# Performance work log

Hardware: AMD Instinct MI355X
Metric: run time of the kernel (lower is better)

Reference implementation:

```python
import jax, jax.numpy as jnp
import numpy as np

N, E, D, H, OUT, L, G = 50000, 800000, 128, 128, 128, 5, 512
EMB = L * H  # 640
BN_EPS = 1e-5


def setup_inputs() -> dict:
    key = jax.random.key(0)
    ks = jax.random.split(key, 24)
    s_h = 1.0 / np.sqrt(H)
    s_e = 1.0 / np.sqrt(EMB)
    inp = {
        'x': jax.random.normal(ks[0], (N, D), jnp.float32),
        'edge_index': jax.random.randint(ks[1], (2, E), 0, N, jnp.int32),
        'batch': jnp.sort(jax.random.randint(ks[2], (N,), 0, G, jnp.int32)),
        # per-layer GINConv MLP: Linear(D/H->H), BN(H), ReLU, Linear(H->H). D==H so stackable.
        'conv_W1': jax.random.normal(ks[3], (L, H, H), jnp.float32) * s_h,
        'conv_b1': jnp.zeros((L, H), jnp.float32),
        'conv_g1': jnp.ones((L, H), jnp.float32),
        'conv_be1': jnp.zeros((L, H), jnp.float32),
        'conv_W2': jax.random.normal(ks[4], (L, H, H), jnp.float32) * s_h,
        'conv_b2': jnp.zeros((L, H), jnp.float32),
        'eps': jnp.zeros((L,), jnp.float32),  # train_eps=True, init 0.0
        # outer BatchNorm per layer
        'bn_g': jnp.ones((L, H), jnp.float32),
        'bn_b': jnp.zeros((L, H), jnp.float32),
        # per-layer prediction heads Linear(H -> OUT)
        'pred_W': jax.random.normal(ks[5], (L, H, OUT), jnp.float32) * s_h,
        'pred_b': jnp.zeros((L, OUT), jnp.float32),
        # global_d FF(EMB): 3 stacked Linear(EMB,EMB) + shortcut
        'gW': jax.random.normal(ks[6], (3, EMB, EMB), jnp.float32) * s_e,
        'gb': jnp.zeros((3, EMB), jnp.float32),
        'gsW': jax.random.normal(ks[7], (EMB, EMB), jnp.float32) * s_e,
        'gsb': jnp.zeros((EMB,), jnp.float32),
        # local_d FF(EMB)
        'lW': jax.random.normal(ks[8], (3, EMB, EMB), jnp.float32) * s_e,
        'lb': jnp.zeros((3, EMB), jnp.float32),
        'lsW': jax.random.normal(ks[9], (EMB, EMB), jnp.float32) * s_e,
        'lsb': jnp.zeros((EMB,), jnp.float32),
    }
    return inp


def _bn(h, g, b):
    # BatchNorm1d, training mode: batch stats over node dim (biased var)
    m = jnp.mean(h, axis=0)
    v = jnp.var(h, axis=0)
    return g * (h - m) * jax.lax.rsqrt(v + BN_EPS) + b


def _ff(x, W, b, Ws, bs):
    h = x
    for i in range(3):
        h = jax.nn.relu(h @ W[i] + b[i])
    return h + x @ Ws + bs


def reference(x, edge_index, batch, conv_W1, conv_b1, conv_g1, conv_be1,
              conv_W2, conv_b2, eps, bn_g, bn_b, pred_W, pred_b,
              gW, gb, gsW, gsb, lW, lb, lsW, lsb):
    src, dst = edge_index[0], edge_index[1]
    h = x
    xs = []
    for i in range(L):
        # GINConv: (1+eps)*x_i + sum_{j->i} x_j, then MLP
        agg = jax.ops.segment_sum(h[src], dst, num_segments=N)
        h = (1.0 + eps[i]) * h + agg
        h = _bn(h @ conv_W1[i] + conv_b1[i], conv_g1[i], conv_be1[i])
        h = jax.nn.relu(h)
        h = h @ conv_W2[i] + conv_b2[i]
        h = jax.nn.relu(_bn(h, bn_g[i], bn_b[i]))
        xs.append(h)
    # per-layer graph sum-pool + prediction head (dropout in eval = identity)
    xpool = [jax.ops.segment_sum(xs[i], batch, num_segments=G) @ pred_W[i] + pred_b[i]
             for i in range(L)]
    xcat = jnp.concatenate(xpool, axis=1)            # [G, L*OUT]
    graph_embedding = _ff(xcat, gW, gb, gsW, gsb)     # [G, EMB]
    node_embedding = _ff(jnp.concatenate(xs, axis=1), lW, lb, lsW, lsb)  # [N, EMB]
    return (graph_embedding, node_embedding, xcat)
```

## Files before the change

### kernel.cpp

```cpp
#include <hip/hip_runtime.h>

constexpr int H    = 128;
constexpr int LNUM = 5;
constexpr int NG   = 512;
constexpr int EMB  = 640;
constexpr float BN_EPS = 1e-5f;

typedef __attribute__((ext_vector_type(8))) short bf16x8;
typedef __attribute__((ext_vector_type(4))) float f32x4;

__device__ inline unsigned short f2bf(float f){
  unsigned u = __builtin_bit_cast(unsigned, f);
  u += 0x7FFF + ((u >> 16) & 1);
  return (unsigned short)(u >> 16);
}
__device__ inline float bf2f(unsigned short h){
  unsigned u = ((unsigned)h) << 16;
  return __builtin_bit_cast(float, u);
}

__device__ inline int xcd_swz(int bid, int nwg){
  int q = nwg >> 3, r = nwg & 7;
  int xcd = bid & 7, idx = bid >> 3;
  return (xcd < r ? xcd*(q+1) : r*(q+1) + (xcd-r)*q) + idx;
}

__global__ void k_zerof(float* p, int n){
  int i = blockIdx.x*256 + threadIdx.x;
  if (i < n) p[i] = 0.f;
}
__global__ void k_zeroi(int* p, int n){
  int i = blockIdx.x*256 + threadIdx.x;
  if (i < n) p[i] = 0;
}

__global__ void k_hist(const int* __restrict__ dst, int E, int* deg){
  int e = blockIdx.x*256 + threadIdx.x;
  if (e < E) atomicAdd(&deg[dst[e]], 1);
}

__global__ __launch_bounds__(1024) void k_scan(int* degcur, int* __restrict__ rowptr, int n){
  __shared__ int wsum[16];
  __shared__ int carry;
  int tid = threadIdx.x, wid = tid >> 6, lane = tid & 63;
  if (tid == 0){ carry = 0; rowptr[0] = 0; }
  __syncthreads();
  for (int base = 0; base < n; base += 1024){
    int v = (base + tid < n) ? degcur[base + tid] : 0;
    int s = v;
#pragma unroll
    for (int off = 1; off < 64; off <<= 1){
      int t = __shfl_up(s, off);
      if (lane >= off) s += t;
    }
    if (lane == 63) wsum[wid] = s;
    __syncthreads();
    if (wid == 0 && lane < 16){
      int wv = wsum[lane];
#pragma unroll
      for (int off = 1; off < 16; off <<= 1){
        int t = __shfl_up(wv, off);
        if (lane >= off) wv += t;
      }
      wsum[lane] = wv;
    }
    __syncthreads();
    int incl = s + (wid ? wsum[wid-1] : 0) + carry;
    if (base + tid < n){ rowptr[base + tid + 1] = incl; degcur[base + tid] = incl - v; }
    __syncthreads();
    if (tid == 0) carry += wsum[15];
    __syncthreads();
  }
}

__global__ void k_scatter(const int* __restrict__ src, const int* __restrict__ dst,
                          int E, int* cursor, int* __restrict__ colsrc){
  int e = blockIdx.x*256 + threadIdx.x;
  if (e < E){
    int d = dst[e];
    int pos = atomicAdd(&cursor[d], 1);
    colsrc[pos] = src[e];
  }
}

__global__ void k_gstart(const int* __restrict__ batch, int N, int* __restrict__ gstart){
  int g = blockIdx.x*256 + threadIdx.x;
  if (g <= NG){
    int lo = 0, hi = N;
    while (lo < hi){
      int mid = (lo + hi) >> 1;
      if (batch[mid] < g) lo = mid + 1; else hi = mid;
    }
    gstart[g] = lo;
  }
}

__global__ void k_castT(const float* __restrict__ W, unsigned short* __restrict__ Wt,
                        int K, int Nn, int ldt, int koff){
  __shared__ float sh[32][33];
  const size_t in_off  = (size_t)blockIdx.z * K * Nn;
  const size_t out_off = (size_t)blockIdx.z * Nn * ldt;
  int n0 = blockIdx.x*32, k0 = blockIdx.y*32;
  int tx = threadIdx.x, ty = threadIdx.y;
  for (int r = ty; r < 32; r += 8)
    sh[r][tx] = W[in_off + (size_t)(k0 + r)*Nn + n0 + tx];
  __syncthreads();
  for (int r = ty; r < 32; r += 8)
    Wt[out_off + (size_t)(n0 + r)*ldt + koff + k0 + tx] = f2bf(sh[tx][r]);
}

__global__ void k_bias2(const float* __restrict__ a, const float* __restrict__ b,
                        float* __restrict__ o){
  int i = threadIdx.x;
  o[i] = a[i] + b[i];
}

__global__ __launch_bounds__(320) void k_pool(const unsigned short* __restrict__ xall,
                                              const int* __restrict__ gstart,
                                              float* __restrict__ pooled){
  int g = blockIdx.x;
  int t = threadIdx.x;
  int n0 = gstart[g], n1 = gstart[g+1];
  float a0 = 0.f, a1 = 0.f;
  for (int n = n0; n < n1; ++n){
    unsigned u = ((const unsigned*)xall)[(size_t)n*(EMB/2) + t];
    a0 += bf2f((unsigned short)u); a1 += bf2f((unsigned short)(u >> 16));
  }
  *(float2*)(pooled + (size_t)g*EMB + 2*t) = make_float2(a0, a1);
}

__global__ __launch_bounds__(128) void k_pred(const float* __restrict__ pooled,
                                              const float* __restrict__ W,
                                              const float* __restrict__ b,
                                              float* __restrict__ xcat){
  int g = blockIdx.x, l = blockIdx.y, o = threadIdx.x;
  __shared__ float sh[128];
  sh[o] = pooled[(size_t)g*EMB + l*H + o];
  __syncthreads();
  const float* Wl = W + (size_t)l*H*H;
  float acc = b[l*H + o];
  for (int k = 0; k < H; ++k) acc = fmaf(sh[k], Wl[k*H + o], acc);
  xcat[(size_t)g*EMB + l*H + o] = acc;
}

template<bool RELU, bool OUT_BF16, bool DUAL>
__global__ __launch_bounds__(512) void k_mm(
    const unsigned short* __restrict__ A, int lda,
    const unsigned short* __restrict__ A2,
    const unsigned short* __restrict__ Bt, int ldb,
    const float* __restrict__ bias,
    void* __restrict__ Cv, int ldc,
    int M, int K)
{
  __shared__ union LdsU {
    unsigned short stage[4][8192];
    unsigned short sc16[128*136];
    float          sc32[128*132];
  } u;
  const int tid  = threadIdx.x;
  const int lane = tid & 63;
  const int w    = tid >> 6;
  const int wr   = w >> 2, wc = w & 3;

  const int nwg = gridDim.x * gridDim.y;
  const int bid = blockIdx.y * gridDim.x + blockIdx.x;
  const int wg  = xcd_swz(bid, nwg);
  const int col0 = (wg % gridDim.x) * 128;
  const int row0 = (wg / gridDim.x) * 128;
  const int KA   = DUAL ? (K >> 1) : K;

  const unsigned short *sA, *sA2p = nullptr, *sB;
  {
    int d = w*1024 + lane*16;
    int m = d >> 6;
    int inner = (d & 63) ^ ((((m >> 1) & 3)) << 4);
    int gm = row0 + m; if (gm > M-1) gm = M-1;
    sA = A + (size_t)gm*lda + (inner >> 1);
    if (DUAL) sA2p = A2 + (size_t)gm*lda + (inner >> 1);
  }
  {
    int d = w*1024 + lane*16;
    int m = d >> 6;
    int inner = (d & 63) ^ ((((m >> 1) & 3)) << 4);
    sB = Bt + (size_t)(col0 + m)*ldb + (inner >> 1);
  }
  const int dAoff = w*1024;
  const int dBoff = 8192 + w*1024;

  f32x4 acc[4][2];
#pragma unroll
  for (int i = 0; i < 4; ++i)
#pragma unroll
    for (int j = 0; j < 2; ++j)
      acc[i][j] = (f32x4){0.f, 0.f, 0.f, 0.f};

  auto STAGE = [&](int buf, int kt){
    int k0 = kt*32, ka = k0;
    bool second = DUAL && (k0 >= KA);
    if (second) ka = k0 - KA;
    char* base = (char*)&u.stage[buf][0];
    const unsigned short* s = second ? (sA2p + ka) : (sA + ka);
    __builtin_amdgcn_global_load_lds(
        (const __attribute__((address_space(1))) void*)s,
        (__attribute__((address_space(3))) void*)(base + dAoff), 16, 0, 0);
    __builtin_amdgcn_global_load_lds(
        (const __attribute__((address_space(1))) void*)(sB + k0),
        (__attribute__((address_space(3))) void*)(base + dBoff), 16, 0, 0);
  };

  auto COMPUTE = [&](int buf){
    const char* Ab = (const char*)&u.stage[buf][0];
    const char* Bb = Ab + 8192;
    const int kb = (lane >> 4) << 4;
    bf16x8 af[4], bfr[2];
#pragma unroll
    for (int i = 0; i < 4; ++i){
      int row = wr*64 + i*16 + (lane & 15);
      af[i] = *(const bf16x8*)(Ab + ((row*64 + kb) ^ ((((row >> 1) & 3)) << 4)));
    }
#pragma unroll
    for (int j = 0; j < 2; ++j){
      int col = wc*32 + j*16 + (lane & 15);
      bfr[j] = *(const bf16x8*)(Bb + ((col*64 + kb) ^ ((((col >> 1) & 3)) << 4)));
    }
#pragma unroll
    for (int i = 0; i < 4; ++i)
#pragma unroll
      for (int j = 0; j < 2; ++j)
        acc[i][j] = __builtin_amdgcn_mfma_f32_16x16x32_bf16(af[i], bfr[j], acc[i][j], 0, 0, 0);
  };

  const int NT = K / 32;
  STAGE(0, 0);
  STAGE(1, 1);
  for (int t = 0; t < NT; ++t){
    if (t + 2 < NT){
      STAGE((t + 2) & 3, t + 2);
      asm volatile("s_waitcnt vmcnt(4)" ::: "memory");
    } else if (t + 1 < NT){
      asm volatile("s_waitcnt vmcnt(2)" ::: "memory");
    } else {
      asm volatile("s_waitcnt vmcnt(0)" ::: "memory");
    }
    __syncthreads();
    COMPUTE(t & 3);
  }

  __syncthreads();
  if (OUT_BF16){
#pragma unroll
    for (int j = 0; j < 2; ++j){
      int cl = wc*32 + j*16 + (lane & 15);
      float bs = bias[col0 + cl];
#pragma unroll
      for (int i = 0; i < 4; ++i){
        int rb = wr*64 + i*16 + ((lane >> 4) << 2);
#pragma unroll
        for (int r = 0; r < 4; ++r){
          float v = acc[i][j][r] + bs;
          if (RELU) v = fmaxf(v, 0.f);
          u.sc16[(rb + r)*136 + cl] = f2bf(v);
        }
      }
    }
    __syncthreads();
    unsigned short* Cb = (unsigned short*)Cv;
    for (int idx = tid; idx < 128*16; idx += 512){
      int rr = idx >> 4, seg = idx & 15;
      int grow = row0 + rr;
      if (grow < M){
        uint4 vv = *(const uint4*)&u.sc16[rr*136 + seg*8];
        *(uint4*)(Cb + (size_t)grow*ldc + col0 + seg*8) = vv;
      }
    }
  } else {
#pragma unroll
    for (int j = 0; j < 2; ++j){
      int cl = wc*32 + j*16 + (lane & 15);
      float bs = bias[col0 + cl];
#pragma unroll
      for (int i = 0; i < 4; ++i){
        int rb = wr*64 + i*16 + ((lane >> 4) << 2);
#pragma unroll
        for (int r = 0; r < 4; ++r){
          float v = acc[i][j][r] + bs;
          if (RELU) v = fmaxf(v, 0.f);
          u.sc32[(rb + r)*132 + cl] = v;
        }
      }
    }
    __syncthreads();
    float* Cf = (float*)Cv;
    for (int idx = tid; idx < 128*32; idx += 512){
      int rr = idx >> 5, seg = idx & 31;
      int grow = row0 + rr;
      if (grow < M){
        float4 vv = *(const float4*)&u.sc32[rr*132 + seg*4];
        *(float4*)(Cf + (size_t)grow*ldc + col0 + seg*4) = vv;
      }
    }
  }
}

template<bool IN_BF16>
__global__ __launch_bounds__(512) void k_mmca(
    const void* __restrict__ hin, int ldh,
    const int* __restrict__ rowptr, const int* __restrict__ colsrc,
    const float* __restrict__ epsp,
    const unsigned short* __restrict__ Bt,
    const float* __restrict__ bias,
    unsigned short* __restrict__ C, int ldc,
    float* __restrict__ sums, float* __restrict__ sumsq,
    int M)
{
  __shared__ unsigned short shm[2*128*128];
  unsigned short* As = shm;
  unsigned short* Bs = shm + 16384;
  const int tid  = threadIdx.x;
  const int lane = tid & 63;
  const int w    = tid >> 6;
  const int wr   = w >> 2, wc = w & 3;

  const int wg   = xcd_swz(blockIdx.x, gridDim.x);
  const int row0 = wg * 128;

#pragma unroll
  for (int j = 0; j < 4; ++j){
    int d = w*4096 + j*1024 + lane*16;
    int m = d >> 8;
    int inner = (d & 255) ^ ((m & 15) << 4);
    __builtin_amdgcn_global_load_lds(
        (const __attribute__((address_space(1))) void*)(Bt + (size_t)m*H + (inner >> 1)),
        (__attribute__((address_space(3))) void*)((char*)Bs + w*4096 + j*1024),
        16, 0, 0);
  }

  {
    int r  = tid >> 2;
    int c0 = (tid & 3) << 5;
    int node = row0 + r; if (node > M-1) node = M-1;
    float ep = 1.0f + *epsp;
    float a[32];
    if (IN_BF16){
      const unsigned short* src = (const unsigned short*)hin + (size_t)node*ldh + c0;
#pragma unroll
      for (int q = 0; q < 4; ++q){
        uint2 v = *(const uint2*)(src + q*8);
        a[q*8+0] = ep*bf2f((unsigned short)v.x);  a[q*8+1] = ep*bf2f((unsigned short)(v.x>>16));
        uint2 v2 = *(const uint2*)(src + q*8 + 4);
        a[q*8+2] = ep*bf2f((unsigned short)v.y);  a[q*8+3] = ep*bf2f((unsigned short)(v.y>>16));
        a[q*8+4] = ep*bf2f((unsigned short)v2.x); a[q*8+5] = ep*bf2f((unsigned short)(v2.x>>16));
        a[q*8+6] = ep*bf2f((unsigned short)v2.y); a[q*8+7] = ep*bf2f((unsigned short)(v2.y>>16));
      }
    } else {
      const float* src = (const float*)hin + (size_t)node*ldh + c0;
#pragma unroll
      for (int q = 0; q < 32; q += 4){
        float4 f = *(const float4*)(src + q);
        a[q] = ep*f.x; a[q+1] = ep*f.y; a[q+2] = ep*f.z; a[q+3] = ep*f.w;
      }
    }
    int e = rowptr[node], e1 = rowptr[node+1];
    for (; e < e1; ++e){
      int s = colsrc[e];
      if (IN_BF16){
        const unsigned short* p = (const unsigned short*)hin + (size_t)s*ldh + c0;
        uint4 v0 = *(const uint4*)(p);
        uint4 v1 = *(const uint4*)(p + 8);
        uint4 v2 = *(const uint4*)(p + 16);
        uint4 v3 = *(const uint4*)(p + 24);
        const unsigned* uu[4] = {(const unsigned*)&v0, (const unsigned*)&v1,
                                 (const unsigned*)&v2, (const unsigned*)&v3};
#pragma unroll
        for (int q = 0; q < 4; ++q)
#pragma unroll
          for (int k = 0; k < 4; ++k){
            unsigned x = uu[q][k];
            a[q*8 + 2*k]     += bf2f((unsigned short)x);
            a[q*8 + 2*k + 1] += bf2f((unsigned short)(x >> 16));
          }
      } else {
        const float* p = (const float*)hin + (size_t)s*ldh + c0;
#pragma unroll
        for (int q = 0; q < 32; q += 4){
          float4 f = *(const float4*)(p + q);
          a[q] += f.x; a[q+1] += f.y; a[q+2] += f.z; a[q+3] += f.w;
        }
      }
    }
#pragma unroll
    for (int q = 0; q < 4; ++q){
      unsigned pk[4];
#pragma unroll
      for (int k = 0; k < 4; ++k)
        pk[k] = (unsigned)f2bf(a[q*8 + 2*k]) | ((unsigned)f2bf(a[q*8 + 2*k + 1]) << 16);
      int byte = (r*256 + (tid & 3)*64 + q*16) ^ ((r & 15) << 4);
      *(uint4*)((char*)As + byte) = *(uint4*)pk;
    }
  }

  asm volatile("s_waitcnt vmcnt(0)" ::: "memory");
  __syncthreads();

  f32x4 acc[4][2];
#pragma unroll
  for (int i = 0; i < 4; ++i)
#pragma unroll
    for (int j = 0; j < 2; ++j)
      acc[i][j] = (f32x4){0.f, 0.f, 0.f, 0.f};

#pragma unroll
  for (int kk = 0; kk < 4; ++kk){
    const int kb = kk*64 + ((lane >> 4) << 4);
    bf16x8 af[4], bfr[2];
#pragma unroll
    for (int i = 0; i < 4; ++i){
      int row = wr*64 + i*16 + (lane & 15);
      af[i] = *(const bf16x8*)((const char*)As + ((row*256 + kb) ^ ((row & 15) << 4)));
    }
#pragma unroll
    for (int j = 0; j < 2; ++j){
      int col = wc*32 + j*16 + (lane & 15);
      bfr[j] = *(const bf16x8*)((const char*)Bs + ((col*256 + kb) ^ ((col & 15) << 4)));
    }
#pragma unroll
    for (int i = 0; i < 4; ++i)
#pragma unroll
      for (int j = 0; j < 2; ++j)
        acc[i][j] = __builtin_amdgcn_mfma_f32_16x16x32_bf16(af[i], bfr[j], acc[i][j], 0, 0, 0);
  }

#pragma unroll
  for (int j = 0; j < 2; ++j){
    int col = wc*32 + j*16 + (lane & 15);
    float bs = bias[col];
    float s = 0.f, q = 0.f;
#pragma unroll
    for (int i = 0; i < 4; ++i){
      int rb = row0 + wr*64 + i*16 + ((lane >> 4) << 2);
#pragma unroll
      for (int r = 0; r < 4; ++r){
        if (rb + r < M){
          float v = acc[i][j][r] + bs;
          s += v; q += v*v;
        }
      }
    }
    s += __shfl_xor(s, 16); q += __shfl_xor(q, 16);
    s += __shfl_xor(s, 32); q += __shfl_xor(q, 32);
    if (lane < 16){
      atomicAdd(&sums[col], s);
      atomicAdd(&sumsq[col], q);
    }
  }

  __syncthreads();
#pragma unroll
  for (int j = 0; j < 2; ++j){
    int cl = wc*32 + j*16 + (lane & 15);
    float bs = bias[cl];
#pragma unroll
    for (int i = 0; i < 4; ++i){
      int rb = wr*64 + i*16 + ((lane >> 4) << 2);
#pragma unroll
      for (int r = 0; r < 4; ++r)
        shm[(rb + r)*136 + cl] = f2bf(acc[i][j][r] + bs);
    }
  }
  __syncthreads();
  for (int idx = tid; idx < 128*16; idx += 512){
    int rr = idx >> 4, seg = idx & 15;
    int grow = row0 + rr;
    if (grow < M){
      uint4 vv = *(const uint4*)&shm[rr*136 + seg*8];
      *(uint4*)(C + (size_t)grow*ldc + seg*8) = vv;
    }
  }
}

__global__ __launch_bounds__(512) void k_mmc2(
    const unsigned short* __restrict__ A,
    const unsigned short* __restrict__ Bt,
    const float* __restrict__ bias,
    const float* __restrict__ statin,
    const float* __restrict__ g1, const float* __restrict__ be1,
    float invn,
    unsigned short* __restrict__ C, int ldc,
    float* __restrict__ sums, float* __restrict__ sumsq,
    int M)
{
  __shared__ unsigned short shm[2*128*128];
  __shared__ float bnsc[128], bnsf[128];
  unsigned short* As = shm;
  unsigned short* Bs = shm + 16384;
  const int tid  = threadIdx.x;
  const int lane = tid & 63;
  const int w    = tid >> 6;
  const int wr   = w >> 2, wc = w & 3;

  const int wg   = xcd_swz(blockIdx.x, gridDim.x);
  const int row0 = wg * 128;

#pragma unroll
  for (int j = 0; j < 4; ++j){
    int d = w*4096 + j*1024 + lane*16;
    int m = d >> 8;
    int inner = (d & 255) ^ ((m & 15) << 4);
    int gm = row0 + m; if (gm > M-1) gm = M-1;
    __builtin_amdgcn_global_load_lds(
        (const __attribute__((address_space(1))) void*)(A + (size_t)gm*H + (inner >> 1)),
        (__attribute__((address_space(3))) void*)((char*)As + w*4096 + j*1024),
        16, 0, 0);
    __builtin_amdgcn_global_load_lds(
        (const __attribute__((address_space(1))) void*)(Bt + (size_t)m*H + (inner >> 1)),
        (__attribute__((address_space(3))) void*)((char*)Bs + w*4096 + j*1024),
        16, 0, 0);
  }

  if (tid < 128){
    float m = statin[tid]*invn;
    float v = statin[128 + tid]*invn - m*m;
    float inv = rsqrtf(v + BN_EPS);
    float sc = g1[tid]*inv;
    bnsc[tid] = sc;
    bnsf[tid] = be1[tid] - m*sc;
  }

  asm volatile("s_waitcnt vmcnt(0)" ::: "memory");
  __syncthreads();

  f32x4 acc[4][2];
#pragma unroll
  for (int i = 0; i < 4; ++i)
#pragma unroll
    for (int j = 0; j < 2; ++j)
      acc[i][j] = (f32x4){0.f, 0.f, 0.f, 0.f};

#pragma unroll
  for (int kk = 0; kk < 4; ++kk){
    const int kb = kk*64 + ((lane >> 4) << 4);
    bf16x8 af[4], bfr[2];
#pragma unroll
    for (int i = 0; i < 4; ++i){
      int row = wr*64 + i*16 + (lane & 15);
      af[i] = *(const bf16x8*)((const char*)As + ((row*256 + kb) ^ ((row & 15) << 4)));
    }
#pragma unroll
    for (int j = 0; j < 2; ++j){
      int col = wc*32 + j*16 + (lane & 15);
      bfr[j] = *(const bf16x8*)((const char*)Bs + ((col*256 + kb) ^ ((col & 15) << 4)));
    }
    {
      int k8 = kk*32 + ((lane >> 4) << 3);
      float4 s0 = *(const float4*)(&bnsc[k8]), s1 = *(const float4*)(&bnsc[k8 + 4]);
      float4 f0 = *(const float4*)(&bnsf[k8]), f1 = *(const float4*)(&bnsf[k8 + 4]);
      float sc[8] = {s0.x,s0.y,s0.z,s0.w,s1.x,s1.y,s1.z,s1.w};
      float sf[8] = {f0.x,f0.y,f0.z,f0.w,f1.x,f1.y,f1.z,f1.w};
#pragma unroll
      for (int i = 0; i < 4; ++i){
        bf16x8 aa = af[i], o;
#pragma unroll
        for (int jj = 0; jj < 8; ++jj){
          float v = fmaxf(fmaf(sc[jj], bf2f((unsigned short)aa[jj]), sf[jj]), 0.f);
          o[jj] = (short)f2bf(v);
        }
        af[i] = o;
      }
    }
#pragma unroll
    for (int i = 0; i < 4; ++i)
#pragma unroll
      for (int j = 0; j < 2; ++j)
        acc[i][j] = __builtin_amdgcn_mfma_f32_16x16x32_bf16(af[i], bfr[j], acc[i][j], 0, 0, 0);
  }

#pragma unroll
  for (int j = 0; j < 2; ++j){
    int col = wc*32 + j*16 + (lane & 15);
    float bs = bias[col];
    float s = 0.f, q = 0.f;
#pragma unroll
    for (int i = 0; i < 4; ++i){
      int rb = row0 + wr*64 + i*16 + ((lane >> 4) << 2);
#pragma unroll
      for (int r = 0; r < 4; ++r){
        if (rb + r < M){
          float v = acc[i][j][r] + bs;
          s += v; q += v*v;
        }
      }
    }
    s += __shfl_xor(s, 16); q += __shfl_xor(q, 16);
    s += __shfl_xor(s, 32); q += __shfl_xor(q, 32);
    if (lane < 16){
      atomicAdd(&sums[col], s);
      atomicAdd(&sumsq[col], q);
    }
  }

  __syncthreads();
#pragma unroll
  for (int j = 0; j < 2; ++j){
    int cl = wc*32 + j*16 + (lane & 15);
    float bs = bias[cl];
#pragma unroll
    for (int i = 0; i < 4; ++i){
      int rb = wr*64 + i*16 + ((lane >> 4) << 2);
#pragma unroll
      for (int r = 0; r < 4; ++r)
        shm[(rb + r)*136 + cl] = f2bf(acc[i][j][r] + bs);
    }
  }
  __syncthreads();
  for (int idx = tid; idx < 128*16; idx += 512){
    int rr = idx >> 4, seg = idx & 15;
    int grow = row0 + rr;
    if (grow < M){
      uint4 vv = *(const uint4*)&shm[rr*136 + seg*8];
      *(uint4*)(C + (size_t)grow*ldc + seg*8) = vv;
    }
  }
}

__global__ __launch_bounds__(256) void k_bnapply(const unsigned short* __restrict__ U,
                                                 const float* __restrict__ statp,
                                                 const float* __restrict__ g,
                                                 const float* __restrict__ b,
                                                 float invn,
                                                 unsigned short* __restrict__ out,
                                                 int ldo, int n){
  int i = blockIdx.x*256 + threadIdx.x;
  int total = n * (H/4);
  if (i < total){
    int r = i >> 5;
    int c4 = (i & 31) << 2;
    float4 sm = *(const float4*)(statp + c4);
    float4 sq = *(const float4*)(statp + 128 + c4);
    float4 gg = *(const float4*)(g + c4);
    float4 bb = *(const float4*)(b + c4);
    float m0 = sm.x*invn, m1 = sm.y*invn, m2 = sm.z*invn, m3 = sm.w*invn;
    float s0 = gg.x*rsqrtf(sq.x*invn - m0*m0 + BN_EPS);
    float s1 = gg.y*rsqrtf(sq.y*invn - m1*m1 + BN_EPS);
    float s2 = gg.z*rsqrtf(sq.z*invn - m2*m2 + BN_EPS);
    float s3 = gg.w*rsqrtf(sq.w*invn - m3*m3 + BN_EPS);
    float f0 = bb.x - m0*s0, f1 = bb.y - m1*s1, f2 = bb.z - m2*s2, f3 = bb.w - m3*s3;
    uint2 up = *(const uint2*)(U + (size_t)r*H + c4);
    float a = fmaxf(fmaf(s0, bf2f((unsigned short)up.x),       f0), 0.f);
    float c = fmaxf(fmaf(s1, bf2f((unsigned short)(up.x>>16)), f1), 0.f);
    float d = fmaxf(fmaf(s2, bf2f((unsigned short)up.y),       f2), 0.f);
    float e = fmaxf(fmaf(s3, bf2f((unsigned short)(up.y>>16)), f3), 0.f);
    uint2 o;
    o.x = (unsigned)f2bf(a) | ((unsigned)f2bf(c) << 16);
    o.y = (unsigned)f2bf(d) | ((unsigned)f2bf(e) << 16);
    *(uint2*)(out + (size_t)r*ldo + c4) = o;
  }
}

template<bool RELU, bool ADD_D>
__global__ __launch_bounds__(256) void k_gemm64(
    const float* __restrict__ A, int lda,
    const float* __restrict__ B, int ldb,
    const float* __restrict__ bias,
    const float* D, int ldd,
    float* C, int ldc,
    int M, int N, int K)
{
  __shared__ float As[32][68];
  __shared__ float Bs[32][64];
  const int tid  = threadIdx.x;
  const int tx   = tid & 15;
  const int ty   = tid >> 4;
  const int row0 = blockIdx.x * 64;
  const int col0 = blockIdx.y * 64;
  const int am = tid >> 3;
  const int ak = (tid & 7) << 2;
  const int bk = tid >> 4;
  const int bn = (tid & 15) << 2;
  float acc[4][4] = {};

  for (int k0 = 0; k0 < K; k0 += 32){
#pragma unroll
    for (int h = 0; h < 2; ++h){
      int m  = am + h*32;
      int gr = row0 + m;
      float4 v = make_float4(0.f, 0.f, 0.f, 0.f);
      if (gr < M) v = *(const float4*)(A + (size_t)gr*lda + k0 + ak);
      As[ak+0][m]=v.x; As[ak+1][m]=v.y; As[ak+2][m]=v.z; As[ak+3][m]=v.w;
    }
#pragma unroll
    for (int h = 0; h < 2; ++h){
      int kk = bk + h*16;
      *(float4*)(&Bs[kk][bn]) = *(const float4*)(B + (size_t)(k0+kk)*ldb + col0 + bn);
    }
    __syncthreads();
#pragma unroll 8
    for (int k = 0; k < 32; ++k){
      float4 a = *(const float4*)(&As[k][ty<<2]);
      float4 b = *(const float4*)(&Bs[k][tx<<2]);
      float av[4] = {a.x,a.y,a.z,a.w};
      float bv[4] = {b.x,b.y,b.z,b.w};
#pragma unroll
      for (int i = 0; i < 4; ++i)
#pragma unroll
        for (int j = 0; j < 4; ++j)
          acc[i][j] = fmaf(av[i], bv[j], acc[i][j]);
    }
    __syncthreads();
  }

  const int col = col0 + (tx<<2);
  float4 bv = *(const float4*)(bias + col);
#pragma unroll
  for (int i = 0; i < 4; ++i){
    int row = row0 + (ty<<2) + i;
    if (row < M){
      float r[4] = {acc[i][0]+bv.x, acc[i][1]+bv.y, acc[i][2]+bv.z, acc[i][3]+bv.w};
      if (RELU){
#pragma unroll
        for (int j = 0; j < 4; ++j) r[j] = fmaxf(r[j], 0.f);
      }
      if (ADD_D){
        float4 d = *(const float4*)(D + (size_t)row*ldd + col);
        r[0]+=d.x; r[1]+=d.y; r[2]+=d.z; r[3]+=d.w;
      }
      *(float4*)(C + (size_t)row*ldc + col) = make_float4(r[0],r[1],r[2],r[3]);
    }
  }
}

extern "C" void kernel_launch(void* const* d_in, const int* in_sizes, int n_in,
                              void* d_out, int out_size, void* d_ws, size_t ws_size,
                              hipStream_t stream) {
  const float* x        = (const float*)d_in[0];
  const int*   ei       = (const int*)d_in[1];
  const int*   batch    = (const int*)d_in[2];
  const float* conv_W1  = (const float*)d_in[3];
  const float* conv_b1  = (const float*)d_in[4];
  const float* conv_g1  = (const float*)d_in[5];
  const float* conv_be1 = (const float*)d_in[6];
  const float* conv_W2  = (const float*)d_in[7];
  const float* conv_b2  = (const float*)d_in[8];
  const float* epsv     = (const float*)d_in[9];
  const float* bn_g     = (const float*)d_in[10];
  const float* bn_b     = (const float*)d_in[11];
  const float* pred_W   = (const float*)d_in[12];
  const float* pred_b   = (const float*)d_in[13];
  const float* gW       = (const float*)d_in[14];
  const float* gb       = (const float*)d_in[15];
  const float* gsW      = (const float*)d_in[16];
  const float* gsb      = (const float*)d_in[17];
  const float* lW       = (const float*)d_in[18];
  const float* lb       = (const float*)d_in[19];
  const float* lsW      = (const float*)d_in[20];
  const float* lsb      = (const float*)d_in[21];

  const int N = in_sizes[0] / H;
  const int E = in_sizes[1] / 2;
  const int* srcI = ei;
  const int* dstI = ei + E;

  float* out = (float*)d_out;
  float* GE = out;
  float* NE = out + (size_t)NG*EMB;
  float* XC = NE + (size_t)N*EMB;

  unsigned short* xall = (unsigned short*)d_ws;
  unsigned short* h1   = xall + (size_t)N*EMB;
  unsigned short* h2   = h1 + (size_t)N*EMB;
  unsigned short* ub   = h1;
  unsigned short* tb   = h1 + (size_t)N*H;

  float* pooled  = (float*)(h2 + (size_t)N*EMB);
  float* gtmp1   = pooled + (size_t)NG*EMB;
  float* gtmp2   = gtmp1 + (size_t)NG*EMB;
  float* slots   = gtmp2 + (size_t)NG*EMB;
  float* biasNE  = slots + 2560;
  unsigned short* W1t   = (unsigned short*)(biasNE + EMB);
  unsigned short* W2t   = W1t + (size_t)LNUM*H*H;
  unsigned short* lWt01 = W2t + (size_t)LNUM*H*H;
  unsigned short* Wcat  = lWt01 + (size_t)2*EMB*EMB;
  int* rowptr = (int*)(Wcat + (size_t)2*EMB*EMB);
  int* cursor = rowptr + (N + 1);
  int* colsrc = cursor + N;
  int* gstart = colsrc + E;

  k_zerof<<<10, 256, 0, stream>>>(slots, 2560);

  k_zeroi<<<(N+255)/256, 256, 0, stream>>>(cursor, N);
  k_hist<<<(E+255)/256, 256, 0, stream>>>(dstI, E, cursor);
  k_scan<<<1, 1024, 0, stream>>>(cursor, rowptr, N);
  k_scatter<<<(E+255)/256, 256, 0, stream>>>(srcI, dstI, E, cursor, colsrc);
  k_gstart<<<(NG+256)/256, 256, 0, stream>>>(batch, N, gstart);

  const dim3 tb32(32, 8);
  k_castT<<<dim3(H/32, H/32, LNUM), tb32, 0, stream>>>(conv_W1, W1t, H, H, H, 0);
  k_castT<<<dim3(H/32, H/32, LNUM), tb32, 0, stream>>>(conv_W2, W2t, H, H, H, 0);
  k_castT<<<dim3(EMB/32, EMB/32, 2), tb32, 0, stream>>>(lW, lWt01, EMB, EMB, EMB, 0);
  k_castT<<<dim3(EMB/32, EMB/32, 1), tb32, 0, stream>>>(lW + (size_t)2*EMB*EMB, Wcat,
                                                        EMB, EMB, 2*EMB, 0);
  k_castT<<<dim3(EMB/32, EMB/32, 1), tb32, 0, stream>>>(lsW, Wcat, EMB, EMB, 2*EMB, EMB);
  k_bias2<<<1, EMB, 0, stream>>>(lb + (size_t)2*EMB, lsb, biasNE);

  const float invn = 1.0f / (float)N;
  const int nrow = (N + 127)/128;

  for (int l = 0; l < LNUM; ++l){
    float* slot1 = slots + (size_t)l*512;
    float* slot2 = slot1 + 256;

    if (l == 0)
      k_mmca<false><<<nrow, 512, 0, stream>>>(
          x, H, rowptr, colsrc, epsv, W1t, conv_b1,
          ub, H, slot1, slot1 + 128, N);
    else
      k_mmca<true><<<nrow, 512, 0, stream>>>(
          xall + (size_t)(l-1)*H, EMB, rowptr, colsrc, epsv + l,
          W1t + (size_t)l*H*H, conv_b1 + l*H,
          ub, H, slot1, slot1 + 128, N);

    k_mmc2<<<nrow, 512, 0, stream>>>(
        ub, W2t + (size_t)l*H*H, conv_b2 + l*H,
        slot1, conv_g1 + l*H, conv_be1 + l*H, invn,
        tb, H, slot2, slot2 + 128, N);

    k_bnapply<<<(N*32 + 255)/256, 256, 0, stream>>>(
        tb, slot2, bn_g + l*H, bn_b + l*H, invn,
        xall + (size_t)l*H, EMB, N);
  }

  k_pool<<<NG, 320, 0, stream>>>(xall, gstart, pooled);
  k_pred<<<dim3(NG, LNUM), 128, 0, stream>>>(pooled, pred_W, pred_b, XC);

  const dim3 gg((NG + 63)/64, EMB/64);
  k_gemm64<false,false><<<gg, 256, 0, stream>>>(XC, EMB, gsW, EMB, gsb,
                                                nullptr, 0, GE, EMB, NG, EMB, EMB);
  k_gemm64<true,false><<<gg, 256, 0, stream>>>(XC, EMB, gW, EMB, gb,
                                               nullptr, 0, gtmp1, EMB, NG, EMB, EMB);
  k_gemm64<true,false><<<gg, 256, 0, stream>>>(gtmp1, EMB, gW + (size_t)EMB*EMB, EMB, gb + EMB,
                                               nullptr, 0, gtmp2, EMB, NG, EMB, EMB);
  k_gemm64<true,true><<<gg, 256, 0, stream>>>(gtmp2, EMB, gW + (size_t)2*EMB*EMB, EMB, gb + 2*EMB,
                                              GE, EMB, GE, EMB, NG, EMB, EMB);

  const dim3 gn(EMB/128, nrow);
  k_mm<true,true,false><<<gn, 512, 0, stream>>>(
      xall, EMB, nullptr, lWt01, EMB, lb, h1, EMB, N, EMB);
  k_mm<true,true,false><<<gn, 512, 0, stream>>>(
      h1, EMB, nullptr, lWt01 + (size_t)EMB*EMB, EMB, lb + EMB, h2, EMB, N, EMB);
  k_mm<false,false,true><<<gn, 512, 0, stream>>>(
      h2, EMB, xall, Wcat, 2*EMB, biasNE, NE, EMB, N, 2*EMB);
}
```

Before: 1.148 ms.

## Enlarge node-FF GEMM tile to 256x128 with K=64 triple-buffered pipeline

The node-embedding GEMM kernel now uses 256x128 output tiles, K steps of 64, and a 3-stage LDS buffer instead of 128x128 tiles with K=32 and 4 stages. Each wave computes a 64x64 sub-tile with 16 accumulators, and it interleaves its prefetch loads with MFMA groups under setprio and sched_barrier. The larger tile gives more reuse per global load and fewer loop iterations. In exchange it uses more LDS and registers, so occupancy drops, the grid has fewer blocks, and every inner step adds extra barriers. The fp32 epilogue is split into two 128-row passes so it fits the scratch buffer.

```diff
diff --git a/kernel.cpp b/kernel.cpp
--- a/kernel.cpp
+++ b/kernel.cpp
@@ -153,111 +153,140 @@
     int M, int K)
 {
   __shared__ union LdsU {
-    unsigned short stage[4][8192];
-    unsigned short sc16[128*136];
+    unsigned short stage[3][24576];
+    unsigned short sc16[256*136];
     float          sc32[128*132];
   } u;
   const int tid  = threadIdx.x;
   const int lane = tid & 63;
   const int w    = tid >> 6;
-  const int wr   = w >> 2, wc = w & 3;
+  const int wrr  = w >> 1;
+  const int wcc  = w & 1;
 
   const int nwg = gridDim.x * gridDim.y;
   const int bid = blockIdx.y * gridDim.x + blockIdx.x;
   const int wg  = xcd_swz(bid, nwg);
   const int col0 = (wg % gridDim.x) * 128;
-  const int row0 = (wg / gridDim.x) * 128;
+  const int row0 = (wg / gridDim.x) * 256;
   const int KA   = DUAL ? (K >> 1) : K;
 
-  const unsigned short *sA, *sA2p = nullptr, *sB;
-  {
-    int d = w*1024 + lane*16;
-    int m = d >> 6;
-    int inner = (d & 63) ^ ((((m >> 1) & 3)) << 4);
+  const unsigned short *sA[4], *sA2p[4], *sB[2];
+  int dA[4], dB[2];
+#pragma unroll
+  for (int j = 0; j < 4; ++j){
+    int d = w*4096 + j*1024 + lane*16;
+    int m = d >> 7;
+    int inner = (d & 127) ^ ((m & 7) << 4);
     int gm = row0 + m; if (gm > M-1) gm = M-1;
-    sA = A + (size_t)gm*lda + (inner >> 1);
-    if (DUAL) sA2p = A2 + (size_t)gm*lda + (inner >> 1);
-  }
-  {
-    int d = w*1024 + lane*16;
-    int m = d >> 6;
-    int inner = (d & 63) ^ ((((m >> 1) & 3)) << 4);
-    sB = Bt + (size_t)(col0 + m)*ldb + (inner >> 1);
-  }
-  const int dAoff = w*1024;
-  const int dBoff = 8192 + w*1024;
-
-  f32x4 acc[4][2];
+    sA[j] = A + (size_t)gm*lda + (inner >> 1);
+    if (DUAL) sA2p[j] = A2 + (size_t)gm*lda + (inner >> 1);
+    dA[j] = w*4096 + j*1024;
+  }
+#pragma unroll
+  for (int j = 0; j < 2; ++j){
+    int d = w*2048 + j*1024 + lane*16;
+    int m = d >> 7;
+    int inner = (d & 127) ^ ((m & 7) << 4);
+    sB[j] = Bt + (size_t)(col0 + m)*ldb + (inner >> 1);
+    dB[j] = 32768 + w*2048 + j*1024;
+  }
+
+  f32x4 acc[4][4];
 #pragma unroll
   for (int i = 0; i < 4; ++i)
 #pragma unroll
-    for (int j = 0; j < 2; ++j)
+    for (int j = 0; j < 4; ++j)
       acc[i][j] = (f32x4){0.f, 0.f, 0.f, 0.f};
 
-  auto STAGE = [&](int buf, int kt){
-    int k0 = kt*32, ka = k0;
-    bool second = DUAL && (k0 >= KA);
-    if (second) ka = k0 - KA;
+  auto STAGE_A = [&](int buf, int kt, int j0){
+    int k0 = kt*64, ka = k0;
+    bool sec = DUAL && (k0 >= KA);
+    if (sec) ka = k0 - KA;
     char* base = (char*)&u.stage[buf][0];
-    const unsigned short* s = second ? (sA2p + ka) : (sA + ka);
-    __builtin_amdgcn_global_load_lds(
-        (const __attribute__((address_space(1))) void*)s,
-        (__attribute__((address_space(3))) void*)(base + dAoff), 16, 0, 0);
-    __builtin_amdgcn_global_load_lds(
-        (const __attribute__((address_space(1))) void*)(sB + k0),
-        (__attribute__((address_space(3))) void*)(base + dBoff), 16, 0, 0);
+#pragma unroll
+    for (int jj = 0; jj < 2; ++jj){
+      const unsigned short* s = sec ? (sA2p[j0+jj] + ka) : (sA[j0+jj] + ka);
+      __builtin_amdgcn_global_load_lds(
+          (const __attribute__((address_space(1))) void*)s,
+          (__attribute__((address_space(3))) void*)(base + dA[j0+jj]), 16, 0, 0);
+    }
   };
-
-  auto COMPUTE = [&](int buf){
-    const char* Ab = (const char*)&u.stage[buf][0];
-    const char* Bb = Ab + 8192;
-    const int kb = (lane >> 4) << 4;
-    bf16x8 af[4], bfr[2];
-#pragma unroll
-    for (int i = 0; i < 4; ++i){
-      int row = wr*64 + i*16 + (lane & 15);
-      af[i] = *(const bf16x8*)(Ab + ((row*64 + kb) ^ ((((row >> 1) & 3)) << 4)));
-    }
-#pragma unroll
-    for (int j = 0; j < 2; ++j){
-      int col = wc*32 + j*16 + (lane & 15);
-      bfr[j] = *(const bf16x8*)(Bb + ((col*64 + kb) ^ ((((col >> 1) & 3)) << 4)));
-    }
-#pragma unroll
-    for (int i = 0; i < 4; ++i)
-#pragma unroll
-      for (int j = 0; j < 2; ++j)
-        acc[i][j] = __builtin_amdgcn_mfma_f32_16x16x32_bf16(af[i], bfr[j], acc[i][j], 0, 0, 0);
+  auto STAGE_B = [&](int buf, int kt){
+    int k0 = kt*64;
+    char* base = (char*)&u.stage[buf][0];
+#pragma unroll
+    for (int jj = 0; jj < 2; ++jj)
+      __builtin_amdgcn_global_load_lds(
+          (const __attribute__((address_space(1))) void*)(sB[jj] + k0),
+          (__attribute__((address_space(3))) void*)(base + dB[jj]), 16, 0, 0);
   };
 
-  const int NT = K / 32;
-  STAGE(0, 0);
-  STAGE(1, 1);
+  const int NT = K / 64;
+  STAGE_A(0, 0, 0); STAGE_A(0, 0, 2); STAGE_B(0, 0);
+  STAGE_A(1, 1, 0); STAGE_A(1, 1, 2); STAGE_B(1, 1);
+  asm volatile("s_waitcnt vmcnt(6)" ::: "memory");
+  __syncthreads();
+
   for (int t = 0; t < NT; ++t){
-    if (t + 2 < NT){
-      STAGE((t + 2) & 3, t + 2);
-      asm volatile("s_waitcnt vmcnt(4)" ::: "memory");
-    } else if (t + 1 < NT){
-      asm volatile("s_waitcnt vmcnt(2)" ::: "memory");
-    } else {
-      asm volatile("s_waitcnt vmcnt(0)" ::: "memory");
-    }
-    __syncthreads();
-    COMPUTE(t & 3);
+    const char* Ab = (const char*)&u.stage[t % 3][0];
+    const char* Bb = Ab + 32768;
+    const int kbq = (lane >> 4) << 4;
+    const bool pre = (t + 2 < NT);
+    const int bufn = (t + 2) % 3;
+    bf16x8 bfr[4][2];
+#pragma unroll
+    for (int ib = 0; ib < 4; ++ib){
+      bf16x8 af0, af1;
+      {
+        int row = wrr*64 + ib*16 + (lane & 15);
+        af0 = *(const bf16x8*)(Ab + ((row*128 + kbq)      ^ ((row & 7) << 4)));
+        af1 = *(const bf16x8*)(Ab + ((row*128 + 64 + kbq) ^ ((row & 7) << 4)));
+      }
+      if (ib == 0){
+#pragma unroll
+        for (int j = 0; j < 4; ++j){
+          int col = wcc*64 + j*16 + (lane & 15);
+          bfr[j][0] = *(const bf16x8*)(Bb + ((col*128 + kbq)      ^ ((col & 7) << 4)));
+          bfr[j][1] = *(const bf16x8*)(Bb + ((col*128 + 64 + kbq) ^ ((col & 7) << 4)));
+        }
+      }
+      if (pre){
+        if (ib == 0) STAGE_A(bufn, t + 2, 0);
+        else if (ib == 1) STAGE_A(bufn, t + 2, 2);
+        else if (ib == 2) STAGE_B(bufn, t + 2);
+      }
+      __syncthreads();
+      asm volatile("s_waitcnt lgkmcnt(0)" ::: "memory");
+      __builtin_amdgcn_sched_barrier(0);
+      __builtin_amdgcn_s_setprio(1);
+#pragma unroll
+      for (int j = 0; j < 4; ++j){
+        acc[ib][j] = __builtin_amdgcn_mfma_f32_16x16x32_bf16(af0, bfr[j][0], acc[ib][j], 0, 0, 0);
+        acc[ib][j] = __builtin_amdgcn_mfma_f32_16x16x32_bf16(af1, bfr[j][1], acc[ib][j], 0, 0, 0);
+      }
+      __builtin_amdgcn_s_setprio(0);
+      __builtin_amdgcn_sched_barrier(0);
+      __syncthreads();
+    }
+    if (t + 1 < NT){
+      if (t + 2 < NT) asm volatile("s_waitcnt vmcnt(6)" ::: "memory");
+      else            asm volatile("s_waitcnt vmcnt(0)" ::: "memory");
+      __syncthreads();
+    }
   }
 
   __syncthreads();
   if (OUT_BF16){
 #pragma unroll
-    for (int j = 0; j < 2; ++j){
-      int cl = wc*32 + j*16 + (lane & 15);
+    for (int j = 0; j < 4; ++j){
+      int cl = wcc*64 + j*16 + (lane & 15);
       float bs = bias[col0 + cl];
 #pragma unroll
-      for (int i = 0; i < 4; ++i){
-        int rb = wr*64 + i*16 + ((lane >> 4) << 2);
+      for (int ib = 0; ib < 4; ++ib){
+        int rb = wrr*64 + ib*16 + ((lane >> 4) << 2);
 #pragma unroll
         for (int r = 0; r < 4; ++r){
-          float v = acc[i][j][r] + bs;
+          float v = acc[ib][j][r] + bs;
           if (RELU) v = fmaxf(v, 0.f);
           u.sc16[(rb + r)*136 + cl] = f2bf(v);
         }
@@ -265,7 +294,7 @@
     }
     __syncthreads();
     unsigned short* Cb = (unsigned short*)Cv;
-    for (int idx = tid; idx < 128*16; idx += 512){
+    for (int idx = tid; idx < 256*16; idx += 512){
       int rr = idx >> 4, seg = idx & 15;
       int grow = row0 + rr;
       if (grow < M){
@@ -274,30 +303,36 @@
       }
     }
   } else {
-#pragma unroll
-    for (int j = 0; j < 2; ++j){
-      int cl = wc*32 + j*16 + (lane & 15);
-      float bs = bias[col0 + cl];
-#pragma unroll
-      for (int i = 0; i < 4; ++i){
-        int rb = wr*64 + i*16 + ((lane >> 4) << 2);
-#pragma unroll
-        for (int r = 0; r < 4; ++r){
-          float v = acc[i][j][r] + bs;
-          if (RELU) v = fmaxf(v, 0.f);
-          u.sc32[(rb + r)*132 + cl] = v;
+    float* Cf = (float*)Cv;
+#pragma unroll
+    for (int p = 0; p < 2; ++p){
+      if ((wrr >> 1) == p){
+#pragma unroll
+        for (int j = 0; j < 4; ++j){
+          int cl = wcc*64 + j*16 + (lane & 15);
+          float bs = bias[col0 + cl];
+#pragma unroll
+          for (int ib = 0; ib < 4; ++ib){
+            int lr = (wrr & 1)*64 + ib*16 + ((lane >> 4) << 2);
+#pragma unroll
+            for (int r = 0; r < 4; ++r){
+              float v = acc[ib][j][r] + bs;
+              if (RELU) v = fmaxf(v, 0.f);
+              u.sc32[(lr + r)*132 + cl] = v;
+            }
+          }
         }
       }
-    }
-    __syncthreads();
-    float* Cf = (float*)Cv;
-    for (int idx = tid; idx < 128*32; idx += 512){
-      int rr = idx >> 5, seg = idx & 31;
-      int grow = row0 + rr;
-      if (grow < M){
-        float4 vv = *(const float4*)&u.sc32[rr*132 + seg*4];
-        *(float4*)(Cf + (size_t)grow*ldc + col0 + seg*4) = vv;
-      }
+      __syncthreads();
+      for (int idx = tid; idx < 128*32; idx += 512){
+        int rr = idx >> 5, seg = idx & 31;
+        int grow = row0 + p*128 + rr;
+        if (grow < M){
+          float4 vv = *(const float4*)&u.sc32[rr*132 + seg*4];
+          *(float4*)(Cf + (size_t)grow*ldc + col0 + seg*4) = vv;
+        }
+      }
+      __syncthreads();
     }
   }
 }
@@ -841,7 +876,8 @@
   k_gemm64<true,true><<<gg, 256, 0, stream>>>(gtmp2, EMB, gW + (size_t)2*EMB*EMB, EMB, gb + 2*EMB,
                                               GE, EMB, GE, EMB, NG, EMB, EMB);
 
-  const dim3 gn(EMB/128, nrow);
+  const int nrow256 = (N + 255)/256;
+  const dim3 gn(EMB/128, nrow256);
   k_mm<true,true,false><<<gn, 512, 0, stream>>>(
       xall, EMB, nullptr, lWt01, EMB, lb, h1, EMB, N, EMB);
   k_mm<true,true,false><<<gn, 512, 0, stream>>>(
```

New measurement: 1.301 ms. +13.4%, slower.

## Use 64-wide K tiles with double-buffered LDS and register-prefetched fragments

Applied to the files above, without the earlier changes.

Doubles the K step of the bf16 MFMA GEMM to 64, switches LDS staging from four 32-wide buffers to two 64-wide buffers with a new XOR swizzle, and loads all fragments into registers before issuing the next stage's global-to-LDS copies into the same buffer. This halves the number of barrier/wait iterations and lets the loads for stage t+2 overlap the MFMAs of stage t. The trade-off is higher register use for the prefetched fragments. It also relies on raw s_barrier ordering against in-flight LDS reads, which could race if the compiler does not wait on them.

```diff
diff --git a/kernel.cpp b/kernel.cpp
--- a/kernel.cpp
+++ b/kernel.cpp
@@ -153,7 +153,7 @@
     int M, int K)
 {
   __shared__ union LdsU {
-    unsigned short stage[4][8192];
+    unsigned short stage[2][2][8192];
     unsigned short sc16[128*136];
     float          sc32[128*132];
   } u;
@@ -169,23 +169,19 @@
   const int row0 = (wg / gridDim.x) * 128;
   const int KA   = DUAL ? (K >> 1) : K;
 
-  const unsigned short *sA, *sA2p = nullptr, *sB;
-  {
-    int d = w*1024 + lane*16;
-    int m = d >> 6;
-    int inner = (d & 63) ^ ((((m >> 1) & 3)) << 4);
+  const unsigned short *sA[2], *sA2p[2], *sB[2];
+  int dOff[2];
+#pragma unroll
+  for (int j = 0; j < 2; ++j){
+    int d = w*2048 + j*1024 + lane*16;
+    int m = d >> 7;
+    int inner = (d & 127) ^ ((m & 7) << 4);
     int gm = row0 + m; if (gm > M-1) gm = M-1;
-    sA = A + (size_t)gm*lda + (inner >> 1);
-    if (DUAL) sA2p = A2 + (size_t)gm*lda + (inner >> 1);
-  }
-  {
-    int d = w*1024 + lane*16;
-    int m = d >> 6;
-    int inner = (d & 63) ^ ((((m >> 1) & 3)) << 4);
-    sB = Bt + (size_t)(col0 + m)*ldb + (inner >> 1);
-  }
-  const int dAoff = w*1024;
-  const int dBoff = 8192 + w*1024;
+    sA[j]  = A + (size_t)gm*lda + (inner >> 1);
+    if (DUAL) sA2p[j] = A2 + (size_t)gm*lda + (inner >> 1);
+    sB[j]  = Bt + (size_t)(col0 + m)*ldb + (inner >> 1);
+    dOff[j] = w*2048 + j*1024;
+  }
 
   f32x4 acc[4][2];
 #pragma unroll
@@ -195,55 +191,65 @@
       acc[i][j] = (f32x4){0.f, 0.f, 0.f, 0.f};
 
   auto STAGE = [&](int buf, int kt){
-    int k0 = kt*32, ka = k0;
+    int k0 = kt*64, ka = k0;
     bool second = DUAL && (k0 >= KA);
     if (second) ka = k0 - KA;
-    char* base = (char*)&u.stage[buf][0];
-    const unsigned short* s = second ? (sA2p + ka) : (sA + ka);
-    __builtin_amdgcn_global_load_lds(
-        (const __attribute__((address_space(1))) void*)s,
-        (__attribute__((address_space(3))) void*)(base + dAoff), 16, 0, 0);
-    __builtin_amdgcn_global_load_lds(
-        (const __attribute__((address_space(1))) void*)(sB + k0),
-        (__attribute__((address_space(3))) void*)(base + dBoff), 16, 0, 0);
+#pragma unroll
+    for (int j = 0; j < 2; ++j){
+      const unsigned short* s = second ? (sA2p[j] + ka) : (sA[j] + ka);
+      __builtin_amdgcn_global_load_lds(
+          (const __attribute__((address_space(1))) void*)s,
+          (__attribute__((address_space(3))) void*)((char*)&u.stage[buf][0][0] + dOff[j]),
+          16, 0, 0);
+    }
+#pragma unroll
+    for (int j = 0; j < 2; ++j)
+      __builtin_amdgcn_global_load_lds(
+          (const __attribute__((address_space(1))) void*)(sB[j] + k0),
+          (__attribute__((address_space(3))) void*)((char*)&u.stage[buf][1][0] + dOff[j]),
+          16, 0, 0);
   };
 
-  auto COMPUTE = [&](int buf){
-    const char* Ab = (const char*)&u.stage[buf][0];
-    const char* Bb = Ab + 8192;
-    const int kb = (lane >> 4) << 4;
-    bf16x8 af[4], bfr[2];
-#pragma unroll
-    for (int i = 0; i < 4; ++i){
-      int row = wr*64 + i*16 + (lane & 15);
-      af[i] = *(const bf16x8*)(Ab + ((row*64 + kb) ^ ((((row >> 1) & 3)) << 4)));
-    }
-#pragma unroll
-    for (int j = 0; j < 2; ++j){
-      int col = wc*32 + j*16 + (lane & 15);
-      bfr[j] = *(const bf16x8*)(Bb + ((col*64 + kb) ^ ((((col >> 1) & 3)) << 4)));
-    }
-#pragma unroll
-    for (int i = 0; i < 4; ++i)
-#pragma unroll
-      for (int j = 0; j < 2; ++j)
-        acc[i][j] = __builtin_amdgcn_mfma_f32_16x16x32_bf16(af[i], bfr[j], acc[i][j], 0, 0, 0);
-  };
-
-  const int NT = K / 32;
+  const int NT = K / 64;
   STAGE(0, 0);
   STAGE(1, 1);
+  asm volatile("s_waitcnt vmcnt(4)" ::: "memory");
+  asm volatile("s_barrier" ::: "memory");
+
   for (int t = 0; t < NT; ++t){
+    const char* Ab = (const char*)&u.stage[t & 1][0][0];
+    const char* Bb = (const char*)&u.stage[t & 1][1][0];
+    bf16x8 af[2][4], bq[2][2];
+#pragma unroll
+    for (int kk = 0; kk < 2; ++kk){
+      const int kb = kk*64 + ((lane >> 4) << 4);
+#pragma unroll
+      for (int i = 0; i < 4; ++i){
+        int row = wr*64 + i*16 + (lane & 15);
+        af[kk][i] = *(const bf16x8*)(Ab + ((row*128 + kb) ^ ((row & 7) << 4)));
+      }
+#pragma unroll
+      for (int j = 0; j < 2; ++j){
+        int col = wc*32 + j*16 + (lane & 15);
+        bq[kk][j] = *(const bf16x8*)(Bb + ((col*128 + kb) ^ ((col & 7) << 4)));
+      }
+    }
     if (t + 2 < NT){
-      STAGE((t + 2) & 3, t + 2);
-      asm volatile("s_waitcnt vmcnt(4)" ::: "memory");
-    } else if (t + 1 < NT){
-      asm volatile("s_waitcnt vmcnt(2)" ::: "memory");
-    } else {
-      asm volatile("s_waitcnt vmcnt(0)" ::: "memory");
-    }
-    __syncthreads();
-    COMPUTE(t & 3);
+      asm volatile("s_barrier" ::: "memory");
+      STAGE(t & 1, t + 2);
+    }
+#pragma unroll
+    for (int kk = 0; kk < 2; ++kk)
+#pragma unroll
+      for (int i = 0; i < 4; ++i)
+#pragma unroll
+        for (int j = 0; j < 2; ++j)
+          acc[i][j] = __builtin_amdgcn_mfma_f32_16x16x32_bf16(af[kk][i], bq[kk][j], acc[i][j], 0, 0, 0);
+    if (t + 1 < NT){
+      if (t + 2 < NT) asm volatile("s_waitcnt vmcnt(4)" ::: "memory");
+      else            asm volatile("s_waitcnt vmcnt(0)" ::: "memory");
+      asm volatile("s_barrier" ::: "memory");
+    }
   }
 
   __syncthreads();
```

Result: faster. 1.074 ms (-6.4%).
